# Performance work log

Hardware: AMD Instinct MI355X
Metric: run time of the kernel (lower is better)

## Reference

```python
import jax, jax.numpy as jnp
import numpy as np

EPS = 1e-5  # BatchNorm1d default eps
E = 64      # embedding_dim
H = 64      # h_dim


def _mlp(x, W1, b1, gamma, beta, W2, b2):
    # Linear -> BatchNorm1d (training-mode batch stats) -> ReLU -> Linear
    h = x @ W1.T + b1
    mu = h.mean(axis=0)
    var = h.var(axis=0)  # biased variance, as BatchNorm normalization uses
    h = jax.nn.relu((h - mu) * jax.lax.rsqrt(var + EPS) * gamma + beta)
    return h @ W2.T + b2


def _lstm_step(h, c, x, Wih, Whh, bih, bhh):
    # PyTorch LSTM gate order: i, f, g, o
    gates = x @ Wih.T + bih + h @ Whh.T + bhh
    i, f, g, o = jnp.split(gates, 4, axis=-1)
    c = jax.nn.sigmoid(f) * c + jax.nn.sigmoid(i) * jnp.tanh(g)
    h = jax.nn.sigmoid(o) * jnp.tanh(c)
    return h, c


def setup_inputs() -> dict:
    key = jax.random.key(0)
    ks = jax.random.split(key, 16)
    OBS_LEN, BATCH = 8, 131072
    f32 = jnp.float32
    inp = {
        "obs_traj": jax.random.uniform(ks[0], (OBS_LEN, BATCH, 2), dtype=f32) * 100.0,
        # spatial_embedding MLP: [2, 16, 64]
        "se_W1": jax.random.normal(ks[1], (16, 2), f32) * 0.5,
        "se_b1": jnp.zeros((16,), f32),
        "se_gamma": jnp.ones((16,), f32),
        "se_beta": jnp.zeros((16,), f32),
        "se_W2": jax.random.normal(ks[2], (E, 16), f32) * 0.2,
        "se_b2": jnp.zeros((E,), f32),
        # hidden2pos MLP: [64, 16, 2]
        "hp_W1": jax.random.normal(ks[3], (16, H), f32) * 0.1,
        "hp_b1": jnp.zeros((16,), f32),
        "hp_gamma": jnp.ones((16,), f32),
        "hp_beta": jnp.zeros((16,), f32),
        "hp_W2": jax.random.normal(ks[4], (2, 16), f32) * 0.2,
        "hp_b2": jnp.zeros((2,), f32),
        # LSTM(64, 64, num_layers=1)
        "Wih": jax.random.normal(ks[5], (4 * H, E), f32) * 0.1,
        "Whh": jax.random.normal(ks[6], (4 * H, H), f32) * 0.1,
        "bih": jnp.zeros((4 * H,), f32),
        "bhh": jnp.zeros((4 * H,), f32),
        "x_max": 100,
        "y_max": 100,
        "pred_len": 12,
    }
    return inp


def reference(obs_traj, se_W1, se_b1, se_gamma, se_beta, se_W2, se_b2,
              hp_W1, hp_b1, hp_gamma, hp_beta, hp_W2, hp_b2,
              Wih, Whh, bih, bhh, x_max, y_max, pred_len):
    T, B, _ = obs_traj.shape
    xy_max = jnp.asarray([x_max, y_max], dtype=obs_traj.dtype)
    obs = obs_traj / xy_max  # (T, B, 2)

    # embed observed trajectory: (T*B, 2) -> (T, B, E)
    emb = _mlp(obs.reshape(-1, 2), se_W1, se_b1, se_gamma, se_beta, se_W2, se_b2)
    emb = emb.reshape(T, B, E)

    h0 = jnp.zeros((B, H), obs.dtype)
    c0 = jnp.zeros((B, H), obs.dtype)

    def enc(carry, x):
        h, c = carry
        h, c = _lstm_step(h, c, x, Wih, Whh, bih, bhh)
        return (h, c), None

    (h, c), _ = jax.lax.scan(enc, (h0, c0), emb)

    def dec(carry, _):
        h, c, last_pos = carry
        pos_rel = _mlp(h, hp_W1, hp_b1, hp_gamma, hp_beta, hp_W2, hp_b2)  # (B, 2)
        # relative_to_abs over a single step == pos_rel + last_pos
        last_pos = jax.nn.sigmoid(pos_rel + last_pos)
        x = _mlp(last_pos, se_W1, se_b1, se_gamma, se_beta, se_W2, se_b2)  # (B, E)
        h, c = _lstm_step(h, c, x, Wih, Whh, bih, bhh)
        return (h, c, last_pos), last_pos

    _, pred = jax.lax.scan(dec, (h, c, obs[-1]), None, length=pred_len)
    return pred * xy_max  # (pred_len, B, 2)
```

## Files before the change

kernel.cpp:

```cpp
#include <hip/hip_runtime.h>
#include <math.h>


#define TT 8
#define PLEN 12
#define ROWS 64
#define NBUCK 16
#define XSTR 104

typedef unsigned short u16;
typedef short short8 __attribute__((ext_vector_type(8)));
typedef float f4 __attribute__((ext_vector_type(4)));
union U8 { u16 u[8]; short8 v; };

#define ST_ENCM 0
#define ST_HP(d)  (128 + (d)*512)
#define ST_MOM(d) (128 + PLEN*512 + (d)*128)
#define ST_TOTAL  (128 + PLEN*512 + PLEN*128)

struct KP {
  const float *obs;
  const float *seW1,*seb1,*seg,*sebeta,*seW2,*seb2;
  const float *hpW1,*hpb1,*hpg,*hpbeta,*hpW2,*hpb2;
  const float *Wih,*Whh,*bih,*bhh;
  const int *xmax,*ymax;
  float *c,*lastpos,*avalg,*M,*gbias,*gbc;
  u16 *Xg1,*Xg2,*Xg3,*W1G,*W2G,*W3G,*H1G,*H2G,*H3G;
  double *stats;
  float *out;
  int B;
};

__device__ __forceinline__ float finv(float d){
  float r = __builtin_amdgcn_rcpf(d);
  return r*(2.f - d*r);
}
__device__ __forceinline__ float sigf(float x){
  float z = fminf(fmaxf(-x, -80.f), 80.f);
  return finv(1.f + __expf(z));
}
__device__ __forceinline__ float tanhf_(float x){
  float z = fminf(fmaxf(2.f*x, -80.f), 80.f);
  return 1.f - 2.f*finv(__expf(z) + 1.f);
}
__device__ __forceinline__ u16 f2bf(float x){
  union{float f; unsigned u;} v; v.f = x;
  unsigned r = v.u + 0x7FFFu + ((v.u >> 16) & 1u);
  return (u16)(r >> 16);
}
__device__ __forceinline__ float bf2f(u16 b){
  union{unsigned u; float f;} v; v.u = ((unsigned)b) << 16; return v.f;
}
__device__ __forceinline__ void split3(float x, u16& a, u16& b, u16& c){
  a = f2bf(x);
  float r1 = x - bf2f(a);
  b = f2bf(r1);
  float r2 = r1 - bf2f(b);
  c = f2bf(r2);
}

#define MF6(A1c,A2c,A3c,b1,b2,b3,accv) \
  accv = __builtin_amdgcn_mfma_f32_16x16x32_bf16(A1c, b1, accv, 0,0,0); \
  accv = __builtin_amdgcn_mfma_f32_16x16x32_bf16(A1c, b2, accv, 0,0,0); \
  accv = __builtin_amdgcn_mfma_f32_16x16x32_bf16(A2c, b1, accv, 0,0,0); \
  accv = __builtin_amdgcn_mfma_f32_16x16x32_bf16(A2c, b2, accv, 0,0,0); \
  accv = __builtin_amdgcn_mfma_f32_16x16x32_bf16(A1c, b3, accv, 0,0,0); \
  accv = __builtin_amdgcn_mfma_f32_16x16x32_bf16(A3c, b1, accv, 0,0,0);

__device__ __forceinline__ void fold_se_mom(const KP& P, const double* stb, double N,
                                            float* sef, int tid){
  if (tid < 16){
    double Sx=0, Sy=0, Sxx=0, Syy=0, Sxy=0;
    for (int b = 0; b < NBUCK; ++b){
      const double* m = stb + b*8;
      Sx += m[0]; Sy += m[1]; Sxx += m[2]; Syy += m[3]; Sxy += m[4];
    }
    double a = (double)P.seW1[2*tid], bb = (double)P.seW1[2*tid+1], cb = (double)P.seb1[tid];
    double S1 = a*Sx + bb*Sy + N*cb;
    double S2 = a*a*Sxx + bb*bb*Syy + 2.0*a*bb*Sxy + 2.0*a*cb*Sx + 2.0*bb*cb*Sy + N*cb*cb;
    double mu = S1/N, var = S2/N - mu*mu;
    float sc = rsqrtf((float)var + 1e-5f) * P.seg[tid];
    float sh = P.sebeta[tid] - (float)mu*sc;
    sef[tid]      = P.seW1[2*tid]*sc;
    sef[16 + tid] = P.seW1[2*tid+1]*sc;
    sef[32 + tid] = P.seb1[tid]*sc + sh;
  }
}

__device__ __forceinline__ void do_epilogue(f4 (&acc)[2][4], float (&cr)[2][4],
                                            u16* X1, u16* X2, u16* X3,
                                            bool first, int lane, int wid){
  const int c = lane & 15, q = lane >> 4;
  #pragma unroll
  for (int ci = 0; ci < 2; ++ci){
    const int j = (2*wid + ci)*4 + q;
    #pragma unroll
    for (int rt = 0; rt < 4; ++rt){
      const int r = rt*16 + c;
      float iv = acc[ci][rt].x, fv = acc[ci][rt].y;
      float gv = acc[ci][rt].z, ov = acc[ci][rt].w;
      float cp = first ? 0.f : cr[ci][rt];
      float cn = sigf(fv)*cp + sigf(iv)*tanhf_(gv);
      cr[ci][rt] = cn;
      float hn = sigf(ov)*tanhf_(cn);
      u16 a, b, cc2;
      split3(hn, a, b, cc2);
      X1[r*XSTR + j] = a; X2[r*XSTR + j] = b; X3[r*XSTR + j] = cc2;
    }
  }
}

__device__ __forceinline__ void tail_xg_aval(const KP& P, long row0,
                                             const u16* X1, const u16* X2, const u16* X3,
                                             double* redd, double* st,
                                             int tid, int lane, int wid, int blk){
  {
    int r = tid >> 3, ch = tid & 7;
    *(short8*)&P.Xg1[(row0 + r)*64 + ch*8] = *(const short8*)&X1[r*XSTR + ch*8];
    *(short8*)&P.Xg2[(row0 + r)*64 + ch*8] = *(const short8*)&X2[r*XSTR + ch*8];
    *(short8*)&P.Xg3[(row0 + r)*64 + ch*8] = *(const short8*)&X3[r*XSTR + ch*8];
  }
  if (wid < 4){
    const int c = lane & 15, q = lane >> 4, rt = wid;
    f4 av = *(const f4*)&P.hpb1[q*4];
    #pragma unroll
    for (int kc = 0; kc < 2; ++kc){
      const int aoff = (lane & 15)*64 + kc*32 + q*8;
      short8 HA1 = *(const short8*)&P.H1G[aoff];
      short8 HA2 = *(const short8*)&P.H2G[aoff];
      short8 HA3 = *(const short8*)&P.H3G[aoff];
      const int boff = (rt*16 + c)*XSTR + kc*32 + q*8;
      short8 b1 = *(const short8*)&X1[boff];
      short8 b2 = *(const short8*)&X2[boff];
      short8 b3 = *(const short8*)&X3[boff];
      MF6(HA1, HA2, HA3, b1, b2, b3, av);
    }
    #pragma unroll
    for (int i = 0; i < 4; ++i)
      P.avalg[(long)(q*4 + i)*P.B + row0 + rt*16 + c] = av[i];
    #pragma unroll
    for (int i = 0; i < 4; ++i){
      double s = (double)av[i];
      double s2 = s*s;
      #pragma unroll
      for (int off = 8; off; off >>= 1){
        s  += __shfl_down(s,  off, 16);
        s2 += __shfl_down(s2, off, 16);
      }
      if (c == 0){
        redd[wid*32 + q*4 + i]      = s;
        redd[wid*32 + 16 + q*4 + i] = s2;
      }
    }
  }
  __syncthreads();
  if (tid < 32){
    double s = redd[tid] + redd[32 + tid] + redd[64 + tid] + redd[96 + tid];
    atomicAdd(&st[(blk & (NBUCK-1))*32 + tid], s);
  }
}

__global__ __launch_bounds__(256) void k_prep(KP P){
  const int g = threadIdx.x;
  {
    const float* __restrict__ wr = P.Wih + g*64;
    double gb = (double)P.bih[g] + (double)P.bhh[g];
    for (int e = 0; e < 64; ++e) gb += (double)wr[e]*(double)P.seb2[e];
    P.gbias[g] = (float)gb;
    for (int q = 0; q < 16; ++q){
      double m = 0.0;
      for (int e = 0; e < 64; ++e) m += (double)wr[e]*(double)P.seW2[e*16+q];
      P.M[g*16+q] = (float)m;
    }
  }
  __syncthreads();
  {
    const int cidx = g, gate = cidx & 3, j = cidx >> 2;
    P.gbc[cidx] = P.gbias[gate*64 + j];
    for (int k = 0; k < 96; ++k){
      float w = 0.f;
      if (k < 64)      w = P.Whh[(gate*64 + j)*64 + k];
      else if (k < 80) w = P.M[(gate*64 + j)*16 + (k - 64)];
      u16 a, b, c;
      split3(w, a, b, c);
      P.W1G[cidx*96 + k] = a;
      P.W2G[cidx*96 + k] = b;
      P.W3G[cidx*96 + k] = c;
    }
    if (cidx < 16){
      for (int k = 0; k < 64; ++k){
        u16 a, b, c;
        split3(P.hpW1[cidx*64 + k], a, b, c);
        P.H1G[cidx*64 + k] = a;
        P.H2G[cidx*64 + k] = b;
        P.H3G[cidx*64 + k] = c;
      }
    }
  }
}

__global__ __launch_bounds__(512) void k_stats_mom(KP P){
  __shared__ double redd[5*9];
  const int tid = threadIdx.x, lane = tid & 63, wid = tid >> 6;
  const int row = blockIdx.x*512 + tid;
  const int B = P.B;
  const float xm = (float)P.xmax[0], ym = (float)P.ymax[0];
  double sx=0, sy=0, sxx=0, syy=0, sxy=0;
  #pragma unroll 1
  for (int t = 0; t < TT; ++t){
    float2 o = ((const float2*)P.obs)[(long)t*B + row];
    float x = o.x/xm, y = o.y/ym;
    sx += (double)x; sy += (double)y;
    sxx += (double)x*(double)x; syy += (double)y*(double)y;
    sxy += (double)x*(double)y;
  }
  #pragma unroll
  for (int off = 32; off; off >>= 1){
    sx  += __shfl_down(sx,  off, 64);
    sy  += __shfl_down(sy,  off, 64);
    sxx += __shfl_down(sxx, off, 64);
    syy += __shfl_down(syy, off, 64);
    sxy += __shfl_down(sxy, off, 64);
  }
  if (lane == 0){
    redd[0*9+wid]=sx; redd[1*9+wid]=sy; redd[2*9+wid]=sxx;
    redd[3*9+wid]=syy; redd[4*9+wid]=sxy;
  }
  __syncthreads();
  if (tid < 5){
    double s = 0.0;
    for (int w = 0; w < 8; ++w) s += redd[tid*9 + w];
    atomicAdd(&P.stats[ST_ENCM + (blockIdx.x & (NBUCK-1))*8 + tid], s);
  }
}

__global__ __launch_bounds__(512) void k_enc(KP P){
  __shared__ __align__(16) u16 X1[ROWS*XSTR];
  __shared__ __align__(16) u16 X2[ROWS*XSTR];
  __shared__ __align__(16) u16 X3[ROWS*XSTR];
  __shared__ float sef[48];
  __shared__ double redd[128];
  const int tid = threadIdx.x, lane = tid & 63, wid = tid >> 6;
  const int B = P.B;
  const long row0 = (long)blockIdx.x * ROWS;
  const float xm = (float)P.xmax[0], ym = (float)P.ymax[0];
  const int c = lane & 15, q = lane >> 4;

  short8 A1r[2][3], A2r[2][3], A3r[2][3];
  f4 biasr[2];
  #pragma unroll
  for (int ci = 0; ci < 2; ++ci){
    const int crow = (2*wid + ci)*16 + c;
    #pragma unroll
    for (int kc = 0; kc < 3; ++kc){
      const int aoff = crow*96 + kc*32 + q*8;
      A1r[ci][kc] = *(const short8*)&P.W1G[aoff];
      A2r[ci][kc] = *(const short8*)&P.W2G[aoff];
      A3r[ci][kc] = *(const short8*)&P.W3G[aoff];
    }
    biasr[ci] = *(const f4*)&P.gbc[(2*wid + ci)*16 + q*4];
  }

  for (int m = tid; m < (ROWS*XSTR)/2; m += 512){
    ((unsigned*)X1)[m] = 0u; ((unsigned*)X2)[m] = 0u; ((unsigned*)X3)[m] = 0u;
  }
  fold_se_mom(P, P.stats + ST_ENCM, 8.0*(double)B, sef, tid);
  __syncthreads();

  if (tid < ROWS){
    float2 o = ((const float2*)P.obs)[row0 + tid];
    float p0 = o.x/xm, p1 = o.y/ym;
    #pragma unroll
    for (int qq = 0; qq < 16; ++qq){
      float tv = sef[qq]*p0 + sef[16+qq]*p1 + sef[32+qq];
      tv = tv > 0.f ? tv : 0.f;
      u16 a, b, cc;
      split3(tv, a, b, cc);
      X1[tid*XSTR + 64 + qq] = a; X2[tid*XSTR + 64 + qq] = b; X3[tid*XSTR + 64 + qq] = cc;
    }
  }
  __syncthreads();

  float cr[2][4];
  f4 acc[2][4];

  #pragma unroll 1
  for (int t = 0; t < TT; ++t){
    #pragma unroll
    for (int ci = 0; ci < 2; ++ci)
      #pragma unroll
      for (int rt = 0; rt < 4; ++rt) acc[ci][rt] = biasr[ci];
    #pragma unroll
    for (int rt = 0; rt < 4; ++rt){
      #pragma unroll
      for (int kc = 0; kc < 3; ++kc){
        const int boff = (rt*16 + c)*XSTR + kc*32 + q*8;
        short8 b1 = *(const short8*)&X1[boff];
        short8 b2 = *(const short8*)&X2[boff];
        short8 b3 = *(const short8*)&X3[boff];
        #pragma unroll
        for (int ci = 0; ci < 2; ++ci){
          MF6(A1r[ci][kc], A2r[ci][kc], A3r[ci][kc], b1, b2, b3, acc[ci][rt]);
        }
      }
    }
    __syncthreads();
    do_epilogue(acc, cr, X1, X2, X3, t == 0, lane, wid);
    if (t < TT-1 && tid < ROWS){
      float2 o = ((const float2*)P.obs)[(long)(t+1)*B + row0 + tid];
      float p0 = o.x/xm, p1 = o.y/ym;
      #pragma unroll
      for (int qq = 0; qq < 16; ++qq){
        float tv = sef[qq]*p0 + sef[16+qq]*p1 + sef[32+qq];
        tv = tv > 0.f ? tv : 0.f;
        u16 a, b, cc;
        split3(tv, a, b, cc);
        X1[tid*XSTR + 64 + qq] = a; X2[tid*XSTR + 64 + qq] = b; X3[tid*XSTR + 64 + qq] = cc;
      }
    }
    __syncthreads();
  }

  #pragma unroll
  for (int ci = 0; ci < 2; ++ci){
    const int j = (2*wid + ci)*4 + q;
    #pragma unroll
    for (int rt = 0; rt < 4; ++rt)
      P.c[(long)j*B + row0 + rt*16 + c] = cr[ci][rt];
  }
  tail_xg_aval(P, row0, X1, X2, X3, redd, P.stats + ST_HP(0), tid, lane, wid, blockIdx.x);
}

template<bool FIRSTD>
__global__ __launch_bounds__(512) void k_dec_pos(KP P, int d){
  __shared__ float hpf[32];
  __shared__ double redd[5*9];
  const int tid = threadIdx.x, lane = tid & 63, wid = tid >> 6;
  const int B = P.B;
  const int row = blockIdx.x*512 + tid;
  if (tid < 16){
    const double* st = P.stats + ST_HP(d);
    double s = 0.0, s2 = 0.0;
    for (int b = 0; b < NBUCK; ++b){ s += st[b*32 + tid]; s2 += st[b*32 + 16 + tid]; }
    double invN = 1.0/(double)B;
    double mu = s*invN, var = s2*invN - mu*mu;
    float sc = rsqrtf((float)var + 1e-5f) * P.hpg[tid];
    hpf[tid] = sc;
    hpf[16+tid] = P.hpbeta[tid] - (float)mu*sc;
  }
  __syncthreads();

  float r0v = P.hpb2[0], r1v = P.hpb2[1];
  #pragma unroll
  for (int qq = 0; qq < 16; ++qq){
    float a = P.avalg[(long)qq*B + row];
    a = a*hpf[qq] + hpf[16+qq];
    a = a > 0.f ? a : 0.f;
    r0v += a*P.hpW2[qq]; r1v += a*P.hpW2[16+qq];
  }
  const float xm = (float)P.xmax[0], ym = (float)P.ymax[0];
  float l0, l1;
  if constexpr (FIRSTD){
    float2 o = ((const float2*)P.obs)[(long)(TT-1)*B + row];
    l0 = o.x/xm; l1 = o.y/ym;
  } else {
    float2 lp = ((const float2*)P.lastpos)[row];
    l0 = lp.x; l1 = lp.y;
  }
  l0 = sigf(r0v + l0);
  l1 = sigf(r1v + l1);
  ((float2*)P.lastpos)[row] = make_float2(l0, l1);
  ((float2*)P.out)[(long)d*B + row] = make_float2(l0*xm, l1*ym);

  double a0=l0, a1=l1, a2=(double)l0*(double)l0, a3=(double)l1*(double)l1, a4=(double)l0*(double)l1;
  #pragma unroll
  for (int off = 32; off; off >>= 1){
    a0 += __shfl_down(a0, off, 64); a1 += __shfl_down(a1, off, 64);
    a2 += __shfl_down(a2, off, 64); a3 += __shfl_down(a3, off, 64);
    a4 += __shfl_down(a4, off, 64);
  }
  if (lane == 0){
    redd[0*9+wid]=a0; redd[1*9+wid]=a1; redd[2*9+wid]=a2;
    redd[3*9+wid]=a3; redd[4*9+wid]=a4;
  }
  __syncthreads();
  if (tid < 5){
    double s = 0.0;
    for (int w = 0; w < 8; ++w) s += redd[tid*9 + w];
    atomicAdd(&P.stats[ST_MOM(d) + (blockIdx.x & (NBUCK-1))*8 + tid], s);
  }
}

template<int DUMMY>
__global__ __launch_bounds__(512) void k_dec_lstm(KP P, int d){
  __shared__ __align__(16) u16 X1[ROWS*XSTR];
  __shared__ __align__(16) u16 X2[ROWS*XSTR];
  __shared__ __align__(16) u16 X3[ROWS*XSTR];
  __shared__ float sef[48];
  __shared__ double redd[128];
  const int tid = threadIdx.x, lane = tid & 63, wid = tid >> 6;
  const int B = P.B;
  const long row0 = (long)blockIdx.x * ROWS;
  const int c = lane & 15, q = lane >> 4;

  fold_se_mom(P, P.stats + ST_MOM(d), (double)B, sef, tid);
  __syncthreads();

  short8 vb1[4], vb2[4], vb3[4];
  {
    const short8 z = {0,0,0,0,0,0,0,0};
    #pragma unroll
    for (int rt = 0; rt < 4; ++rt){ vb1[rt] = z; vb2[rt] = z; vb3[rt] = z; }
    if (q < 2){
      #pragma unroll
      for (int rt = 0; rt < 4; ++rt){
        float2 lp = ((const float2*)P.lastpos)[row0 + rt*16 + c];
        U8 u1, u2, u3;
        #pragma unroll
        for (int j = 0; j < 8; ++j){
          const int ch = q*8 + j;
          float tv = sef[ch]*lp.x + sef[16+ch]*lp.y + sef[32+ch];
          tv = tv > 0.f ? tv : 0.f;
          split3(tv, u1.u[j], u2.u[j], u3.u[j]);
        }
        vb1[rt] = u1.v; vb2[rt] = u2.v; vb3[rt] = u3.v;
      }
    }
  }
  float cr[2][4];
  #pragma unroll
  for (int ci = 0; ci < 2; ++ci){
    const int j = (2*wid + ci)*4 + q;
    #pragma unroll
    for (int rt = 0; rt < 4; ++rt)
      cr[ci][rt] = P.c[(long)j*B + row0 + rt*16 + c];
  }

  f4 acc[2][4];
  #pragma unroll
  for (int ci = 0; ci < 2; ++ci){
    f4 bias = *(const f4*)&P.gbc[(2*wid + ci)*16 + q*4];
    #pragma unroll
    for (int rt = 0; rt < 4; ++rt) acc[ci][rt] = bias;
  }
  #pragma unroll
  for (int rt = 0; rt < 4; ++rt){
    const long gb = (row0 + rt*16 + c)*64;
    #pragma unroll
    for (int kc = 0; kc < 2; ++kc){
      short8 b1 = *(const short8*)&P.Xg1[gb + kc*32 + q*8];
      short8 b2 = *(const short8*)&P.Xg2[gb + kc*32 + q*8];
      short8 b3 = *(const short8*)&P.Xg3[gb + kc*32 + q*8];
      #pragma unroll
      for (int ci = 0; ci < 2; ++ci){
        const int aoff = ((2*wid + ci)*16 + c)*96 + kc*32 + q*8;
        short8 A1 = *(const short8*)&P.W1G[aoff];
        short8 A2 = *(const short8*)&P.W2G[aoff];
        short8 A3 = *(const short8*)&P.W3G[aoff];
        MF6(A1, A2, A3, b1, b2, b3, acc[ci][rt]);
      }
    }
    #pragma unroll
    for (int ci = 0; ci < 2; ++ci){
      const int aoff = ((2*wid + ci)*16 + c)*96 + 2*32 + q*8;
      short8 A1 = *(const short8*)&P.W1G[aoff];
      short8 A2 = *(const short8*)&P.W2G[aoff];
      short8 A3 = *(const short8*)&P.W3G[aoff];
      MF6(A1, A2, A3, vb1[rt], vb2[rt], vb3[rt], acc[ci][rt]);
    }
  }

  do_epilogue(acc, cr, X1, X2, X3, false, lane, wid);
  #pragma unroll
  for (int ci = 0; ci < 2; ++ci){
    const int j = (2*wid + ci)*4 + q;
    #pragma unroll
    for (int rt = 0; rt < 4; ++rt)
      P.c[(long)j*B + row0 + rt*16 + c] = cr[ci][rt];
  }
  __syncthreads();
  tail_xg_aval(P, row0, X1, X2, X3, redd, P.stats + ST_HP(d+1), tid, lane, wid, blockIdx.x);
}

extern "C" void kernel_launch(void* const* d_in, const int* in_sizes, int n_in,
                              void* d_out, int out_size, void* d_ws, size_t ws_size,
                              hipStream_t stream){
  KP P;
  P.obs    = (const float*)d_in[0];
  P.seW1   = (const float*)d_in[1];
  P.seb1   = (const float*)d_in[2];
  P.seg    = (const float*)d_in[3];
  P.sebeta = (const float*)d_in[4];
  P.seW2   = (const float*)d_in[5];
  P.seb2   = (const float*)d_in[6];
  P.hpW1   = (const float*)d_in[7];
  P.hpb1   = (const float*)d_in[8];
  P.hpg    = (const float*)d_in[9];
  P.hpbeta = (const float*)d_in[10];
  P.hpW2   = (const float*)d_in[11];
  P.hpb2   = (const float*)d_in[12];
  P.Wih    = (const float*)d_in[13];
  P.Whh    = (const float*)d_in[14];
  P.bih    = (const float*)d_in[15];
  P.bhh    = (const float*)d_in[16];
  P.xmax   = (const int*)d_in[17];
  P.ymax   = (const int*)d_in[18];

  const int B = in_sizes[0] / (TT*2);
  P.B = B;
  float* ws = (float*)d_ws;
  P.Xg1     = (u16*)(ws);
  P.Xg2     = (u16*)(ws + (size_t)32*B);
  P.c       = ws + (size_t)64*B;
  P.lastpos = ws + (size_t)128*B;
  P.Xg3     = (u16*)(ws + (size_t)130*B);
  P.avalg   = ws + (size_t)162*B;
  float* tail = ws + (size_t)178*B;
  P.M     = tail;
  P.gbias = tail + 4096;
  P.gbc   = tail + 4352;
  P.W1G   = (u16*)(tail + 4608);
  P.W2G   = (u16*)(tail + 4608 + 12288);
  P.W3G   = (u16*)(tail + 4608 + 24576);
  P.H1G   = (u16*)(tail + 4608 + 36864);
  P.H2G   = (u16*)(tail + 4608 + 37376);
  P.H3G   = (u16*)(tail + 4608 + 37888);
  P.stats = (double*)(tail + 4608 + 38400);
  P.out   = (float*)d_out;

  hipMemsetAsync(P.stats, 0, ST_TOTAL*sizeof(double), stream);

  k_prep     <<<1, 256, 0, stream>>>(P);
  k_stats_mom<<<B/512, 512, 0, stream>>>(P);
  k_enc      <<<B/ROWS, 512, 0, stream>>>(P);

  for (int d = 0; d < PLEN; ++d){
    if (d == 0) k_dec_pos<true ><<<B/512, 512, 0, stream>>>(P, d);
    else        k_dec_pos<false><<<B/512, 512, 0, stream>>>(P, d);
    if (d < PLEN-1) k_dec_lstm<0><<<B/ROWS, 512, 0, stream>>>(P, d);
  }
}
```

Before: 1.853 ms.

## Fuse decoder steps into one persistent kernel with grid barriers

Replaces the 23 per-step decoder launches (position MLP and LSTM kernels) with a single persistent kernel of B/512 blocks. Blocks are synchronised by a software grid barrier built on atomics, and each block handles 512 rows in 8 tiles of 64. Last positions and the spatial-embedding inputs stay in LDS across steps, and part of the split-bf16 LSTM weights stays in registers. This targets launch overhead and repeated global round trips, but adds barrier spin cost. It also relies on all 256 blocks being co-resident; otherwise the barrier deadlocks.

Result: slower. 2.592 ms (+39.8%).

```diff
diff --git a/kernel.cpp b/kernel.cpp
--- a/kernel.cpp
+++ b/kernel.cpp
@@ -5,8 +5,12 @@
 #define TT 8
 #define PLEN 12
 #define ROWS 64
+#define DROWS 512
+#define NTILE (DROWS/ROWS)
 #define NBUCK 16
 #define XSTR 104
+#define XSTR2 72
+#define VSTR 16
 
 typedef unsigned short u16;
 typedef short short8 __attribute__((ext_vector_type(8)));
@@ -27,6 +31,7 @@
   float *c,*lastpos,*avalg,*M,*gbias,*gbc;
   u16 *Xg1,*Xg2,*Xg3,*W1G,*W2G,*W3G,*H1G,*H2G,*H3G;
   double *stats;
+  unsigned *bar;
   float *out;
   int B;
 };
@@ -57,6 +62,27 @@
   b = f2bf(r1);
   float r2 = r1 - bf2f(b);
   c = f2bf(r2);
+}
+__device__ __forceinline__ double ald(const double* p){
+  return __hip_atomic_load(p, __ATOMIC_RELAXED, __HIP_MEMORY_SCOPE_AGENT);
+}
+
+__device__ __forceinline__ void grid_barrier(unsigned* bar, int tid){
+  __threadfence();
+  __syncthreads();
+  if (tid == 0){
+    unsigned gen = __hip_atomic_load(bar+1, __ATOMIC_RELAXED, __HIP_MEMORY_SCOPE_AGENT);
+    unsigned a = __hip_atomic_fetch_add(bar, 1u, __ATOMIC_ACQ_REL, __HIP_MEMORY_SCOPE_AGENT);
+    if (a == gridDim.x - 1u){
+      __hip_atomic_store(bar, 0u, __ATOMIC_RELAXED, __HIP_MEMORY_SCOPE_AGENT);
+      __hip_atomic_store(bar+1, gen+1u, __ATOMIC_RELEASE, __HIP_MEMORY_SCOPE_AGENT);
+    } else {
+      while (__hip_atomic_load(bar+1, __ATOMIC_ACQUIRE, __HIP_MEMORY_SCOPE_AGENT) == gen){
+        __builtin_amdgcn_s_sleep(8);
+      }
+    }
+  }
+  __syncthreads();
 }
 
 #define MF6(A1c,A2c,A3c,b1,b2,b3,accv) \
@@ -73,7 +99,7 @@
     double Sx=0, Sy=0, Sxx=0, Syy=0, Sxy=0;
     for (int b = 0; b < NBUCK; ++b){
       const double* m = stb + b*8;
-      Sx += m[0]; Sy += m[1]; Sxx += m[2]; Syy += m[3]; Sxy += m[4];
+      Sx += ald(m+0); Sy += ald(m+1); Sxx += ald(m+2); Syy += ald(m+3); Sxy += ald(m+4);
     }
     double a = (double)P.seW1[2*tid], bb = (double)P.seW1[2*tid+1], cb = (double)P.seb1[tid];
     double S1 = a*Sx + bb*Sy + N*cb;
@@ -87,6 +113,7 @@
   }
 }
 
+template<int STR>
 __device__ __forceinline__ void do_epilogue(f4 (&acc)[2][4], float (&cr)[2][4],
                                             u16* X1, u16* X2, u16* X3,
                                             bool first, int lane, int wid){
@@ -105,20 +132,21 @@
       float hn = sigf(ov)*tanhf_(cn);
       u16 a, b, cc2;
       split3(hn, a, b, cc2);
-      X1[r*XSTR + j] = a; X2[r*XSTR + j] = b; X3[r*XSTR + j] = cc2;
-    }
-  }
-}
-
+      X1[r*STR + j] = a; X2[r*STR + j] = b; X3[r*STR + j] = cc2;
+    }
+  }
+}
+
+template<int STR>
 __device__ __forceinline__ void tail_xg_aval(const KP& P, long row0,
                                              const u16* X1, const u16* X2, const u16* X3,
                                              double* redd, double* st,
                                              int tid, int lane, int wid, int blk){
   {
     int r = tid >> 3, ch = tid & 7;
-    *(short8*)&P.Xg1[(row0 + r)*64 + ch*8] = *(const short8*)&X1[r*XSTR + ch*8];
-    *(short8*)&P.Xg2[(row0 + r)*64 + ch*8] = *(const short8*)&X2[r*XSTR + ch*8];
-    *(short8*)&P.Xg3[(row0 + r)*64 + ch*8] = *(const short8*)&X3[r*XSTR + ch*8];
+    *(short8*)&P.Xg1[(row0 + r)*64 + ch*8] = *(const short8*)&X1[r*STR + ch*8];
+    *(short8*)&P.Xg2[(row0 + r)*64 + ch*8] = *(const short8*)&X2[r*STR + ch*8];
+    *(short8*)&P.Xg3[(row0 + r)*64 + ch*8] = *(const short8*)&X3[r*STR + ch*8];
   }
   if (wid < 4){
     const int c = lane & 15, q = lane >> 4, rt = wid;
@@ -129,7 +157,7 @@
       short8 HA1 = *(const short8*)&P.H1G[aoff];
       short8 HA2 = *(const short8*)&P.H2G[aoff];
       short8 HA3 = *(const short8*)&P.H3G[aoff];
-      const int boff = (rt*16 + c)*XSTR + kc*32 + q*8;
+      const int boff = (rt*16 + c)*STR + kc*32 + q*8;
       short8 b1 = *(const short8*)&X1[boff];
       short8 b2 = *(const short8*)&X2[boff];
       short8 b3 = *(const short8*)&X3[boff];
@@ -305,7 +333,7 @@
       }
     }
     __syncthreads();
-    do_epilogue(acc, cr, X1, X2, X3, t == 0, lane, wid);
+    do_epilogue<XSTR>(acc, cr, X1, X2, X3, t == 0, lane, wid);
     if (t < TT-1 && tid < ROWS){
       float2 o = ((const float2*)P.obs)[(long)(t+1)*B + row0 + tid];
       float p0 = o.x/xm, p1 = o.y/ym;
@@ -328,158 +356,234 @@
     for (int rt = 0; rt < 4; ++rt)
       P.c[(long)j*B + row0 + rt*16 + c] = cr[ci][rt];
   }
-  tail_xg_aval(P, row0, X1, X2, X3, redd, P.stats + ST_HP(0), tid, lane, wid, blockIdx.x);
-}
-
-template<bool FIRSTD>
-__global__ __launch_bounds__(512) void k_dec_pos(KP P, int d){
-  __shared__ float hpf[32];
-  __shared__ double redd[5*9];
+  tail_xg_aval<XSTR>(P, row0, X1, X2, X3, redd, P.stats + ST_HP(0), tid, lane, wid, blockIdx.x);
+}
+
+__global__ __launch_bounds__(512, 2) void k_dec_fused(KP P){
+  __shared__ __align__(16) u16 Xt1[ROWS*XSTR2];
+  __shared__ __align__(16) u16 Xt2[ROWS*XSTR2];
+  __shared__ __align__(16) u16 Xt3[ROWS*XSTR2];
+  __shared__ __align__(16) u16 V1[DROWS*VSTR];
+  __shared__ __align__(16) u16 V2[DROWS*VSTR];
+  __shared__ __align__(16) u16 V3[DROWS*VSTR];
+  __shared__ float2 lp[DROWS];
+  __shared__ float sef[48];
+  __shared__ double redd[128];
+
   const int tid = threadIdx.x, lane = tid & 63, wid = tid >> 6;
   const int B = P.B;
-  const int row = blockIdx.x*512 + tid;
-  if (tid < 16){
-    const double* st = P.stats + ST_HP(d);
-    double s = 0.0, s2 = 0.0;
-    for (int b = 0; b < NBUCK; ++b){ s += st[b*32 + tid]; s2 += st[b*32 + 16 + tid]; }
-    double invN = 1.0/(double)B;
-    double mu = s*invN, var = s2*invN - mu*mu;
-    float sc = rsqrtf((float)var + 1e-5f) * P.hpg[tid];
-    hpf[tid] = sc;
-    hpf[16+tid] = P.hpbeta[tid] - (float)mu*sc;
-  }
-  __syncthreads();
-
-  float r0v = P.hpb2[0], r1v = P.hpb2[1];
-  #pragma unroll
-  for (int qq = 0; qq < 16; ++qq){
-    float a = P.avalg[(long)qq*B + row];
-    a = a*hpf[qq] + hpf[16+qq];
-    a = a > 0.f ? a : 0.f;
-    r0v += a*P.hpW2[qq]; r1v += a*P.hpW2[16+qq];
-  }
+  const long row0 = (long)blockIdx.x * DROWS;
+  const int c = lane & 15, q = lane >> 4;
   const float xm = (float)P.xmax[0], ym = (float)P.ymax[0];
-  float l0, l1;
-  if constexpr (FIRSTD){
-    float2 o = ((const float2*)P.obs)[(long)(TT-1)*B + row];
-    l0 = o.x/xm; l1 = o.y/ym;
-  } else {
-    float2 lp = ((const float2*)P.lastpos)[row];
-    l0 = lp.x; l1 = lp.y;
-  }
-  l0 = sigf(r0v + l0);
-  l1 = sigf(r1v + l1);
-  ((float2*)P.lastpos)[row] = make_float2(l0, l1);
-  ((float2*)P.out)[(long)d*B + row] = make_float2(l0*xm, l1*ym);
-
-  double a0=l0, a1=l1, a2=(double)l0*(double)l0, a3=(double)l1*(double)l1, a4=(double)l0*(double)l1;
-  #pragma unroll
-  for (int off = 32; off; off >>= 1){
-    a0 += __shfl_down(a0, off, 64); a1 += __shfl_down(a1, off, 64);
-    a2 += __shfl_down(a2, off, 64); a3 += __shfl_down(a3, off, 64);
-    a4 += __shfl_down(a4, off, 64);
-  }
-  if (lane == 0){
-    redd[0*9+wid]=a0; redd[1*9+wid]=a1; redd[2*9+wid]=a2;
-    redd[3*9+wid]=a3; redd[4*9+wid]=a4;
-  }
-  __syncthreads();
-  if (tid < 5){
-    double s = 0.0;
-    for (int w = 0; w < 8; ++w) s += redd[tid*9 + w];
-    atomicAdd(&P.stats[ST_MOM(d) + (blockIdx.x & (NBUCK-1))*8 + tid], s);
-  }
-}
-
-template<int DUMMY>
-__global__ __launch_bounds__(512) void k_dec_lstm(KP P, int d){
-  __shared__ __align__(16) u16 X1[ROWS*XSTR];
-  __shared__ __align__(16) u16 X2[ROWS*XSTR];
-  __shared__ __align__(16) u16 X3[ROWS*XSTR];
-  __shared__ float sef[48];
-  __shared__ double redd[128];
-  const int tid = threadIdx.x, lane = tid & 63, wid = tid >> 6;
-  const int B = P.B;
-  const long row0 = (long)blockIdx.x * ROWS;
-  const int c = lane & 15, q = lane >> 4;
-
-  fold_se_mom(P, P.stats + ST_MOM(d), (double)B, sef, tid);
-  __syncthreads();
-
-  short8 vb1[4], vb2[4], vb3[4];
-  {
-    const short8 z = {0,0,0,0,0,0,0,0};
-    #pragma unroll
-    for (int rt = 0; rt < 4; ++rt){ vb1[rt] = z; vb2[rt] = z; vb3[rt] = z; }
-    if (q < 2){
-      #pragma unroll
-      for (int rt = 0; rt < 4; ++rt){
-        float2 lp = ((const float2*)P.lastpos)[row0 + rt*16 + c];
-        U8 u1, u2, u3;
-        #pragma unroll
-        for (int j = 0; j < 8; ++j){
-          const int ch = q*8 + j;
-          float tv = sef[ch]*lp.x + sef[16+ch]*lp.y + sef[32+ch];
-          tv = tv > 0.f ? tv : 0.f;
-          split3(tv, u1.u[j], u2.u[j], u3.u[j]);
-        }
-        vb1[rt] = u1.v; vb2[rt] = u2.v; vb3[rt] = u3.v;
-      }
-    }
-  }
-  float cr[2][4];
+
+  short8 A1r[2][3], A2r[2][3];
+  f4 biasr[2];
   #pragma unroll
   for (int ci = 0; ci < 2; ++ci){
-    const int j = (2*wid + ci)*4 + q;
-    #pragma unroll
-    for (int rt = 0; rt < 4; ++rt)
-      cr[ci][rt] = P.c[(long)j*B + row0 + rt*16 + c];
-  }
-
-  f4 acc[2][4];
-  #pragma unroll
-  for (int ci = 0; ci < 2; ++ci){
-    f4 bias = *(const f4*)&P.gbc[(2*wid + ci)*16 + q*4];
-    #pragma unroll
-    for (int rt = 0; rt < 4; ++rt) acc[ci][rt] = bias;
-  }
-  #pragma unroll
-  for (int rt = 0; rt < 4; ++rt){
-    const long gb = (row0 + rt*16 + c)*64;
-    #pragma unroll
-    for (int kc = 0; kc < 2; ++kc){
-      short8 b1 = *(const short8*)&P.Xg1[gb + kc*32 + q*8];
-      short8 b2 = *(const short8*)&P.Xg2[gb + kc*32 + q*8];
-      short8 b3 = *(const short8*)&P.Xg3[gb + kc*32 + q*8];
+    const int crow = (2*wid + ci)*16 + c;
+    #pragma unroll
+    for (int kc = 0; kc < 3; ++kc){
+      const int aoff = crow*96 + kc*32 + q*8;
+      A1r[ci][kc] = *(const short8*)&P.W1G[aoff];
+      A2r[ci][kc] = *(const short8*)&P.W2G[aoff];
+    }
+    biasr[ci] = *(const f4*)&P.gbc[(2*wid + ci)*16 + q*4];
+  }
+
+  #pragma unroll 1
+  for (int d = 0; d < PLEN; ++d){
+    if (tid < 16){
+      const double* st = P.stats + ST_HP(d);
+      double s = 0.0, s2 = 0.0;
+      for (int b = 0; b < NBUCK; ++b){ s += ald(&st[b*32 + tid]); s2 += ald(&st[b*32 + 16 + tid]); }
+      double invN = 1.0/(double)B;
+      double mu = s*invN, var = s2*invN - mu*mu;
+      float sc = rsqrtf((float)var + 1e-5f) * P.hpg[tid];
+      sef[tid] = sc;
+      sef[16+tid] = P.hpbeta[tid] - (float)mu*sc;
+    }
+    __syncthreads();
+    double a0, a1, a2, a3, a4;
+    {
+      const long row = row0 + tid;
+      float r0v = P.hpb2[0], r1v = P.hpb2[1];
+      #pragma unroll
+      for (int qq = 0; qq < 16; ++qq){
+        float a = P.avalg[(long)qq*B + row];
+        a = a*sef[qq] + sef[16+qq];
+        a = a > 0.f ? a : 0.f;
+        r0v += a*P.hpW2[qq]; r1v += a*P.hpW2[16+qq];
+      }
+      float l0, l1;
+      if (d == 0){
+        float2 o = ((const float2*)P.obs)[(long)(TT-1)*B + row];
+        l0 = o.x/xm; l1 = o.y/ym;
+      } else {
+        float2 t = lp[tid]; l0 = t.x; l1 = t.y;
+      }
+      l0 = sigf(r0v + l0);
+      l1 = sigf(r1v + l1);
+      lp[tid] = make_float2(l0, l1);
+      ((float2*)P.out)[(long)d*B + row] = make_float2(l0*xm, l1*ym);
+      a0 = l0; a1 = l1;
+      a2 = (double)l0*(double)l0; a3 = (double)l1*(double)l1; a4 = (double)l0*(double)l1;
+    }
+    #pragma unroll
+    for (int off = 32; off; off >>= 1){
+      a0 += __shfl_down(a0, off, 64); a1 += __shfl_down(a1, off, 64);
+      a2 += __shfl_down(a2, off, 64); a3 += __shfl_down(a3, off, 64);
+      a4 += __shfl_down(a4, off, 64);
+    }
+    if (lane == 0){
+      redd[0*9+wid]=a0; redd[1*9+wid]=a1; redd[2*9+wid]=a2;
+      redd[3*9+wid]=a3; redd[4*9+wid]=a4;
+    }
+    __syncthreads();
+    if (tid < 5){
+      double s = 0.0;
+      #pragma unroll
+      for (int w = 0; w < 8; ++w) s += redd[tid*9 + w];
+      atomicAdd(&P.stats[ST_MOM(d) + (blockIdx.x & (NBUCK-1))*8 + tid], s);
+    }
+    if (d == PLEN-1) break;
+    grid_barrier(P.bar, tid);
+
+    fold_se_mom(P, P.stats + ST_MOM(d), (double)B, sef, tid);
+    __syncthreads();
+    {
+      float2 l = lp[tid];
+      U8 u1a, u1b, u2a, u2b, u3a, u3b;
+      #pragma unroll
+      for (int ch = 0; ch < 8; ++ch){
+        float tv = sef[ch]*l.x + sef[16+ch]*l.y + sef[32+ch];
+        tv = tv > 0.f ? tv : 0.f;
+        split3(tv, u1a.u[ch], u2a.u[ch], u3a.u[ch]);
+      }
+      #pragma unroll
+      for (int ch = 8; ch < 16; ++ch){
+        float tv = sef[ch]*l.x + sef[16+ch]*l.y + sef[32+ch];
+        tv = tv > 0.f ? tv : 0.f;
+        split3(tv, u1b.u[ch-8], u2b.u[ch-8], u3b.u[ch-8]);
+      }
+      *(short8*)&V1[tid*VSTR]     = u1a.v;
+      *(short8*)&V1[tid*VSTR + 8] = u1b.v;
+      *(short8*)&V2[tid*VSTR]     = u2a.v;
+      *(short8*)&V2[tid*VSTR + 8] = u2b.v;
+      *(short8*)&V3[tid*VSTR]     = u3a.v;
+      *(short8*)&V3[tid*VSTR + 8] = u3b.v;
+    }
+    __syncthreads();
+
+    #pragma unroll 1
+    for (int tile = 0; tile < NTILE; ++tile){
+      const long trow0 = row0 + tile*ROWS;
+      {
+        const int r = tid >> 3, ch = tid & 7;
+        *(short8*)&Xt1[r*XSTR2 + ch*8] = *(const short8*)&P.Xg1[(trow0 + r)*64 + ch*8];
+        *(short8*)&Xt2[r*XSTR2 + ch*8] = *(const short8*)&P.Xg2[(trow0 + r)*64 + ch*8];
+        *(short8*)&Xt3[r*XSTR2 + ch*8] = *(const short8*)&P.Xg3[(trow0 + r)*64 + ch*8];
+      }
+      float crt[2][4];
       #pragma unroll
       for (int ci = 0; ci < 2; ++ci){
-        const int aoff = ((2*wid + ci)*16 + c)*96 + kc*32 + q*8;
-        short8 A1 = *(const short8*)&P.W1G[aoff];
-        short8 A2 = *(const short8*)&P.W2G[aoff];
-        short8 A3 = *(const short8*)&P.W3G[aoff];
-        MF6(A1, A2, A3, b1, b2, b3, acc[ci][rt]);
-      }
-    }
-    #pragma unroll
-    for (int ci = 0; ci < 2; ++ci){
-      const int aoff = ((2*wid + ci)*16 + c)*96 + 2*32 + q*8;
-      short8 A1 = *(const short8*)&P.W1G[aoff];
-      short8 A2 = *(const short8*)&P.W2G[aoff];
-      short8 A3 = *(const short8*)&P.W3G[aoff];
-      MF6(A1, A2, A3, vb1[rt], vb2[rt], vb3[rt], acc[ci][rt]);
-    }
-  }
-
-  do_epilogue(acc, cr, X1, X2, X3, false, lane, wid);
-  #pragma unroll
-  for (int ci = 0; ci < 2; ++ci){
-    const int j = (2*wid + ci)*4 + q;
-    #pragma unroll
-    for (int rt = 0; rt < 4; ++rt)
-      P.c[(long)j*B + row0 + rt*16 + c] = cr[ci][rt];
-  }
-  __syncthreads();
-  tail_xg_aval(P, row0, X1, X2, X3, redd, P.stats + ST_HP(d+1), tid, lane, wid, blockIdx.x);
+        const int j = (2*wid + ci)*4 + q;
+        #pragma unroll
+        for (int rt = 0; rt < 4; ++rt)
+          crt[ci][rt] = P.c[(long)j*B + trow0 + rt*16 + c];
+      }
+      __syncthreads();
+
+      f4 acc[2][4];
+      #pragma unroll
+      for (int ci = 0; ci < 2; ++ci)
+        #pragma unroll
+        for (int rt = 0; rt < 4; ++rt) acc[ci][rt] = biasr[ci];
+      #pragma unroll
+      for (int rt = 0; rt < 4; ++rt){
+        #pragma unroll
+        for (int kc = 0; kc < 2; ++kc){
+          const int boff = (rt*16 + c)*XSTR2 + kc*32 + q*8;
+          short8 b1 = *(const short8*)&Xt1[boff];
+          short8 b2 = *(const short8*)&Xt2[boff];
+          short8 b3 = *(const short8*)&Xt3[boff];
+          #pragma unroll
+          for (int ci = 0; ci < 2; ++ci){
+            short8 A3 = *(const short8*)&P.W3G[((2*wid + ci)*16 + c)*96 + kc*32 + q*8];
+            MF6(A1r[ci][kc], A2r[ci][kc], A3, b1, b2, b3, acc[ci][rt]);
+          }
+        }
+        short8 vb1 = {0,0,0,0,0,0,0,0}, vb2 = vb1, vb3 = vb1;
+        if (q < 2){
+          const int voff = (tile*ROWS + rt*16 + c)*VSTR + q*8;
+          vb1 = *(const short8*)&V1[voff];
+          vb2 = *(const short8*)&V2[voff];
+          vb3 = *(const short8*)&V3[voff];
+        }
+        #pragma unroll
+        for (int ci = 0; ci < 2; ++ci){
+          short8 A3 = *(const short8*)&P.W3G[((2*wid + ci)*16 + c)*96 + 64 + q*8];
+          MF6(A1r[ci][2], A2r[ci][2], A3, vb1, vb2, vb3, acc[ci][rt]);
+        }
+      }
+      __syncthreads();
+
+      do_epilogue<XSTR2>(acc, crt, Xt1, Xt2, Xt3, false, lane, wid);
+      #pragma unroll
+      for (int ci = 0; ci < 2; ++ci){
+        const int j = (2*wid + ci)*4 + q;
+        #pragma unroll
+        for (int rt = 0; rt < 4; ++rt)
+          P.c[(long)j*B + trow0 + rt*16 + c] = crt[ci][rt];
+      }
+      __syncthreads();
+
+      {
+        const int r = tid >> 3, ch = tid & 7;
+        *(short8*)&P.Xg1[(trow0 + r)*64 + ch*8] = *(const short8*)&Xt1[r*XSTR2 + ch*8];
+        *(short8*)&P.Xg2[(trow0 + r)*64 + ch*8] = *(const short8*)&Xt2[r*XSTR2 + ch*8];
+        *(short8*)&P.Xg3[(trow0 + r)*64 + ch*8] = *(const short8*)&Xt3[r*XSTR2 + ch*8];
+      }
+      if (wid < 4){
+        const int rt = wid;
+        f4 av = *(const f4*)&P.hpb1[q*4];
+        #pragma unroll
+        for (int kc = 0; kc < 2; ++kc){
+          const int aoff = (lane & 15)*64 + kc*32 + q*8;
+          short8 HA1 = *(const short8*)&P.H1G[aoff];
+          short8 HA2 = *(const short8*)&P.H2G[aoff];
+          short8 HA3 = *(const short8*)&P.H3G[aoff];
+          const int boff = (rt*16 + c)*XSTR2 + kc*32 + q*8;
+          short8 b1 = *(const short8*)&Xt1[boff];
+          short8 b2 = *(const short8*)&Xt2[boff];
+          short8 b3 = *(const short8*)&Xt3[boff];
+          MF6(HA1, HA2, HA3, b1, b2, b3, av);
+        }
+        #pragma unroll
+        for (int i = 0; i < 4; ++i)
+          P.avalg[(long)(q*4 + i)*B + trow0 + rt*16 + c] = av[i];
+        #pragma unroll
+        for (int i = 0; i < 4; ++i){
+          double s = (double)av[i], s2 = s*s;
+          #pragma unroll
+          for (int off = 8; off; off >>= 1){
+            s  += __shfl_down(s,  off, 16);
+            s2 += __shfl_down(s2, off, 16);
+          }
+          if (c == 0){
+            redd[wid*32 + q*4 + i]      = s;
+            redd[wid*32 + 16 + q*4 + i] = s2;
+          }
+        }
+      }
+      __syncthreads();
+      if (tid < 32){
+        double s = redd[tid] + redd[32 + tid] + redd[64 + tid] + redd[96 + tid];
+        atomicAdd(&P.stats[ST_HP(d+1) + (blockIdx.x & (NBUCK-1))*32 + tid], s);
+      }
+      __syncthreads();
+    }
+    grid_barrier(P.bar, tid);
+  }
 }
 
 extern "C" void kernel_launch(void* const* d_in, const int* in_sizes, int n_in,
@@ -526,17 +630,13 @@
   P.H2G   = (u16*)(tail + 4608 + 37376);
   P.H3G   = (u16*)(tail + 4608 + 37888);
   P.stats = (double*)(tail + 4608 + 38400);
+  P.bar   = (unsigned*)(P.stats + ST_TOTAL);
   P.out   = (float*)d_out;
 
-  hipMemsetAsync(P.stats, 0, ST_TOTAL*sizeof(double), stream);
+  hipMemsetAsync(P.stats, 0, ST_TOTAL*sizeof(double) + 16, stream);
 
   k_prep     <<<1, 256, 0, stream>>>(P);
   k_stats_mom<<<B/512, 512, 0, stream>>>(P);
   k_enc      <<<B/ROWS, 512, 0, stream>>>(P);
-
-  for (int d = 0; d < PLEN; ++d){
-    if (d == 0) k_dec_pos<true ><<<B/512, 512, 0, stream>>>(P, d);
-    else        k_dec_pos<false><<<B/512, 512, 0, stream>>>(P, d);
-    if (d < PLEN-1) k_dec_lstm<0><<<B/ROWS, 512, 0, stream>>>(P, d);
-  }
-}
+  k_dec_fused<<<B/DROWS, 512, 0, stream>>>(P);
+}
```
